# Performance work log

Hardware: AMD Instinct MI355X
Metric: run time of the kernel (lower is better)

The kernel has to match this reference:

```python
import jax, jax.numpy as jnp
import numpy as np

B, T, MAX_ITEMS = 128, 50, 32
NUM_PRODUCT, E, EW = 100000, 128, 16
D = E + EW  # rnn input/hidden size


def setup_inputs() -> dict:
    key = jax.random.key(0)
    ks = jax.random.split(key, 10)
    # items: 0 is padding; keep roughly half the slots padded (ragged baskets)
    items = jax.random.randint(ks[0], (B, T, MAX_ITEMS), 1, NUM_PRODUCT)
    keep = jax.random.uniform(ks[1], (B, T, MAX_ITEMS)) < 0.5
    keep = keep.at[:, :, 0].set(True)  # at least one item per basket
    items = jnp.where(keep, items, 0)
    flag = jax.random.randint(ks[2], (B, T, 1), 0, 2)
    x = jnp.concatenate([items, flag], axis=-1)  # [B,T,MAX_ITEMS+1], last col = flag
    lengths = jnp.full((B,), T, dtype=jnp.int64)
    hidden = jnp.zeros((1, B, D), dtype=jnp.float32)
    s_e = 1.0 / np.sqrt(E)
    s_d = 1.0 / np.sqrt(D)
    encode_w = jax.random.uniform(ks[3], (NUM_PRODUCT, E), minval=-0.1, maxval=0.1)
    encode_w = encode_w.at[0].set(0.0)  # padding_idx=0
    wchange_w = jax.random.normal(ks[4], (2, EW)) * 0.1
    wchange_w = wchange_w.at[0].set(0.0)  # padding_idx=0
    w_ih = jax.random.uniform(ks[5], (3 * D, D), minval=-s_d, maxval=s_d)
    w_hh = jax.random.uniform(ks[6], (3 * D, D), minval=-s_d, maxval=s_d)
    b_ih = jax.random.uniform(ks[7], (3 * D,), minval=-s_d, maxval=s_d)
    b_hh = jax.random.uniform(ks[8], (3 * D,), minval=-s_d, maxval=s_d)
    fc_w = jax.random.uniform(ks[9], (E, D), minval=-s_d, maxval=s_d)
    fc_b = jnp.zeros((E,), dtype=jnp.float32)
    return {"x": x, "lengths": lengths, "hidden": hidden,
            "encode_w": encode_w, "wchange_w": wchange_w,
            "w_ih": w_ih, "w_hh": w_hh, "b_ih": b_ih, "b_hh": b_hh,
            "fc_w": fc_w, "fc_b": fc_b}


def _embed_baskets(x, encode_w, wchange_w):
    items = x[..., :-1]                      # [B,T,I] product ids, 0 = pad
    flag = x[..., -1]                        # [B,T] 0/1 weight-change flag
    emb = encode_w[items]                    # [B,T,I,E] fused ragged gather
    mask = (items != 0).astype(emb.dtype)[..., None]
    cnt = jnp.maximum(mask.sum(axis=2), 1.0)
    pooled = (emb * mask).sum(axis=2) / cnt  # avg pool over real items [B,T,E]
    w = wchange_w[flag]                      # [B,T,EW]
    return jnp.concatenate([pooled, w], axis=-1)  # [B,T,D]


def _gru(seq, h0, w_ih, w_hh, b_ih, b_hh):
    # seq: [B,T,D], h0: [B,D]; torch GRU cell math
    def step(h, x_t):
        gi = x_t @ w_ih.T + b_ih             # [B,3D]
        gh = h @ w_hh.T + b_hh
        i_r, i_z, i_n = jnp.split(gi, 3, axis=-1)
        h_r, h_z, h_n = jnp.split(gh, 3, axis=-1)
        r = jax.nn.sigmoid(i_r + h_r)
        z = jax.nn.sigmoid(i_z + h_z)
        n = jnp.tanh(i_n + r * h_n)
        h_new = (1.0 - z) * n + z * h
        return h_new, h_new
    h_last, outs = jax.lax.scan(step, h0, jnp.swapaxes(seq, 0, 1))
    return jnp.swapaxes(outs, 0, 1), h_last  # [B,T,D], [B,D]


def reference(x, lengths, hidden, encode_w, wchange_w, w_ih, w_hh, b_ih, b_hh, fc_w, fc_b):
    seq = _embed_baskets(x, encode_w, wchange_w)         # [B,T,D]
    out, h_last = _gru(seq, hidden[0], w_ih, w_hh, b_ih, b_hh)
    dynamic_user = out @ fc_w.T + fc_b                   # [B,T,E]
    return dynamic_user, h_last[None]                    # h_u: [1,B,D]
```

## Files before the change

kernel.cpp:

```cpp
#include <hip/hip_runtime.h>
#include <math.h>

#define B_   128
#define T_   50
#define MI_  32
#define E_   128
#define EW_  16
#define D_   144
#define G_   432
#define N_   (B_*T_)

__global__ __launch_bounds__(128) void embed_kernel(
    const int* __restrict__ x,
    const float* __restrict__ encode_w,
    const float* __restrict__ wchange_w,
    float* __restrict__ seq)
{
    int n = blockIdx.x;
    int tid = threadIdx.x;
    __shared__ int xi[33];
    if (tid < 33) xi[tid] = x[n * 33 + tid];
    __syncthreads();

    float acc = 0.f;
    float cnt = 0.f;
    #pragma unroll
    for (int i = 0; i < MI_; ++i) {
        int it = xi[i];
        if (it != 0) {
            cnt += 1.f;
            acc += encode_w[it * E_ + tid];
        }
    }
    seq[n * D_ + tid] = acc / fmaxf(cnt, 1.f);
    if (tid < EW_) {
        int flag = xi[32];
        seq[n * D_ + E_ + tid] = wchange_w[flag * EW_ + tid];
    }
}

#define GK   144
#define GBK  48
#define GPAD 68

__global__ __launch_bounds__(256) void gemm_bias_kernel(
    const float* __restrict__ A,
    const float* __restrict__ Bw,
    const float* __restrict__ bias,
    float* __restrict__ C,
    int M, int N)
{
    __shared__ float As[GBK * GPAD];
    __shared__ float Bs[GBK * GPAD];

    int tid = threadIdx.x;
    int row0 = blockIdx.x * 64;
    int col0 = blockIdx.y * 64;
    int tx = tid & 15;
    int ty = tid >> 4;

    float acc[4][4] = {};

    int sr = tid >> 2;
    int skq0 = tid & 3;

    for (int k0 = 0; k0 < GK; k0 += GBK) {
        __syncthreads();
        #pragma unroll
        for (int i = 0; i < 3; ++i) {
            int kq = skq0 + i * 4;
            float4 a = *(const float4*)&A[(size_t)(row0 + sr) * GK + k0 + kq * 4];
            int nrow = col0 + sr;
            float4 b = make_float4(0.f, 0.f, 0.f, 0.f);
            if (nrow < N)
                b = *(const float4*)&Bw[(size_t)nrow * GK + k0 + kq * 4];
            As[(kq * 4 + 0) * GPAD + sr] = a.x;
            As[(kq * 4 + 1) * GPAD + sr] = a.y;
            As[(kq * 4 + 2) * GPAD + sr] = a.z;
            As[(kq * 4 + 3) * GPAD + sr] = a.w;
            Bs[(kq * 4 + 0) * GPAD + sr] = b.x;
            Bs[(kq * 4 + 1) * GPAD + sr] = b.y;
            Bs[(kq * 4 + 2) * GPAD + sr] = b.z;
            Bs[(kq * 4 + 3) * GPAD + sr] = b.w;
        }
        __syncthreads();

        #pragma unroll 4
        for (int k = 0; k < GBK; ++k) {
            float4 a4 = *(const float4*)&As[k * GPAD + ty * 4];
            float4 b4 = *(const float4*)&Bs[k * GPAD + tx * 4];
            float av[4] = {a4.x, a4.y, a4.z, a4.w};
            float bv[4] = {b4.x, b4.y, b4.z, b4.w};
            #pragma unroll
            for (int i = 0; i < 4; ++i)
                #pragma unroll
                for (int j = 0; j < 4; ++j)
                    acc[i][j] = fmaf(av[i], bv[j], acc[i][j]);
        }
    }

    int c = col0 + tx * 4;
    if (c < N) {
        float4 bb = *(const float4*)&bias[c];
        #pragma unroll
        for (int i = 0; i < 4; ++i) {
            int r = row0 + ty * 4 + i;
            float4 o;
            o.x = acc[i][0] + bb.x;
            o.y = acc[i][1] + bb.y;
            o.z = acc[i][2] + bb.z;
            o.w = acc[i][3] + bb.w;
            *(float4*)&C[(size_t)r * N + c] = o;
        }
    }
}

__global__ __launch_bounds__(448, 1) void gru_kernel(
    const float* __restrict__ gi,
    const float* __restrict__ w_hh,
    const float* __restrict__ b_hh,
    const float* __restrict__ h0,
    float* __restrict__ hseq,
    float* __restrict__ hlast)
{
    int b = blockIdx.x;
    int tid = threadIdx.x;

    __shared__ __align__(16) float h[D_];
    __shared__ float gh[G_];

    int jrow = (tid < G_) ? tid : (G_ - 1);
    float4 w[36];
    #pragma unroll
    for (int i = 0; i < 36; ++i)
        w[i] = *(const float4*)&w_hh[(size_t)jrow * D_ + i * 4];
    float gbias = b_hh[jrow];

    if (tid < D_) h[tid] = h0[b * D_ + tid];
    __syncthreads();

    for (int t = 0; t < T_; ++t) {
        int n = b * T_ + t;
        float gir = 0.f, giz = 0.f, gin = 0.f;
        if (tid < D_) {
            gir = gi[(size_t)n * G_ + tid];
            giz = gi[(size_t)n * G_ + D_ + tid];
            gin = gi[(size_t)n * G_ + 2 * D_ + tid];
        }

        if (tid < G_) {
            float a0 = 0.f, a1 = 0.f, a2 = 0.f, a3 = 0.f;
            #pragma unroll
            for (int i = 0; i < 36; i += 4) {
                float4 hv0 = *(const float4*)&h[(i + 0) * 4];
                float4 hv1 = *(const float4*)&h[(i + 1) * 4];
                float4 hv2 = *(const float4*)&h[(i + 2) * 4];
                float4 hv3 = *(const float4*)&h[(i + 3) * 4];
                a0 = fmaf(w[i + 0].x, hv0.x, a0); a0 = fmaf(w[i + 0].y, hv0.y, a0);
                a0 = fmaf(w[i + 0].z, hv0.z, a0); a0 = fmaf(w[i + 0].w, hv0.w, a0);
                a1 = fmaf(w[i + 1].x, hv1.x, a1); a1 = fmaf(w[i + 1].y, hv1.y, a1);
                a1 = fmaf(w[i + 1].z, hv1.z, a1); a1 = fmaf(w[i + 1].w, hv1.w, a1);
                a2 = fmaf(w[i + 2].x, hv2.x, a2); a2 = fmaf(w[i + 2].y, hv2.y, a2);
                a2 = fmaf(w[i + 2].z, hv2.z, a2); a2 = fmaf(w[i + 2].w, hv2.w, a2);
                a3 = fmaf(w[i + 3].x, hv3.x, a3); a3 = fmaf(w[i + 3].y, hv3.y, a3);
                a3 = fmaf(w[i + 3].z, hv3.z, a3); a3 = fmaf(w[i + 3].w, hv3.w, a3);
            }
            gh[tid] = ((a0 + a1) + (a2 + a3)) + gbias;
        }
        __syncthreads();

        if (tid < D_) {
            float r = 1.f / (1.f + __expf(-(gir + gh[tid])));
            float z = 1.f / (1.f + __expf(-(giz + gh[D_ + tid])));
            float narg = gin + r * gh[2 * D_ + tid];
            narg = fminf(fmaxf(narg, -15.f), 15.f);
            float e2 = __expf(-2.f * narg);
            float nn = (1.f - e2) / (1.f + e2);
            float hn = (1.f - z) * nn + z * h[tid];
            hseq[(size_t)n * D_ + tid] = hn;
            h[tid] = hn;
        }
        __syncthreads();
    }

    if (tid < D_) hlast[b * D_ + tid] = h[tid];
}

extern "C" void kernel_launch(void* const* d_in, const int* in_sizes, int n_in,
                              void* d_out, int out_size, void* d_ws, size_t ws_size,
                              hipStream_t stream)
{
    const int*   x         = (const int*)d_in[0];
    const float* hidden    = (const float*)d_in[2];
    const float* encode_w  = (const float*)d_in[3];
    const float* wchange_w = (const float*)d_in[4];
    const float* w_ih      = (const float*)d_in[5];
    const float* w_hh      = (const float*)d_in[6];
    const float* b_ih      = (const float*)d_in[7];
    const float* b_hh      = (const float*)d_in[8];
    const float* fc_w      = (const float*)d_in[9];
    const float* fc_b      = (const float*)d_in[10];

    float* out = (float*)d_out;
    float* ws  = (float*)d_ws;
    float* seq  = ws;
    float* gi   = ws + 921600;
    float* hseq = ws + 921600 + 2764800;

    embed_kernel<<<N_, 128, 0, stream>>>(x, encode_w, wchange_w, seq);

    gemm_bias_kernel<<<dim3(N_ / 64, (G_ + 63) / 64), 256, 0, stream>>>(
        seq, w_ih, b_ih, gi, N_, G_);

    gru_kernel<<<B_, 448, 0, stream>>>(gi, w_hh, b_hh, hidden, hseq,
                                       out + (size_t)N_ * E_);

    gemm_bias_kernel<<<dim3(N_ / 64, E_ / 64), 256, 0, stream>>>(
        hseq, fc_w, fc_b, out, N_, E_);
}
```

Before: 212.7 us.

## Split GRU recurrent matvec across 8-lane groups with DPP reductions

The recurrent h·W_hh matvec in the GRU kernel is restructured. Instead of one thread computing a full 144-length dot product per gate row, each group of 8 lanes now handles 6 rows, and each lane covers a 20-element slice of k. Partial sums are combined with DPP cross-lane adds, and the block grows from 448 to 576 threads. This shortens the serial per-step FMA chain on the latency-bound recurrence, at the cost of extra reduction instructions, 120 weight registers per thread, and zero-padded k work.

```diff
diff --git a/kernel.cpp b/kernel.cpp
--- a/kernel.cpp
+++ b/kernel.cpp
@@ -115,7 +115,13 @@
     }
 }
 
-__global__ __launch_bounds__(448, 1) void gru_kernel(
+template<int CTRL>
+__device__ __forceinline__ float dpp_xor_add(float x) {
+    int y = __builtin_amdgcn_mov_dpp(__float_as_int(x), CTRL, 0xF, 0xF, true);
+    return x + __int_as_float(y);
+}
+
+__global__ __launch_bounds__(576) void gru_kernel(
     const float* __restrict__ gi,
     const float* __restrict__ w_hh,
     const float* __restrict__ b_hh,
@@ -125,18 +131,31 @@
 {
     int b = blockIdx.x;
     int tid = threadIdx.x;
-
-    __shared__ __align__(16) float h[D_];
+    int g = tid >> 3;
+    int s = tid & 7;
+    int k0 = s * 20;
+
+    __shared__ __align__(16) float h[160];
     __shared__ float gh[G_];
 
-    int jrow = (tid < G_) ? tid : (G_ - 1);
-    float4 w[36];
+    float w[6][20];
     #pragma unroll
-    for (int i = 0; i < 36; ++i)
-        w[i] = *(const float4*)&w_hh[(size_t)jrow * D_ + i * 4];
-    float gbias = b_hh[jrow];
-
-    if (tid < D_) h[tid] = h0[b * D_ + tid];
+    for (int r = 0; r < 6; ++r) {
+        const float* wrow = &w_hh[(size_t)(6 * g + r) * D_];
+        #pragma unroll
+        for (int q = 0; q < 5; ++q) {
+            int k = k0 + 4 * q;
+            float4 t = make_float4(0.f, 0.f, 0.f, 0.f);
+            if (k < D_) t = *(const float4*)&wrow[k];
+            w[r][4 * q + 0] = t.x;
+            w[r][4 * q + 1] = t.y;
+            w[r][4 * q + 2] = t.z;
+            w[r][4 * q + 3] = t.w;
+        }
+    }
+    float bias = (s < 6) ? b_hh[6 * g + s] : 0.f;
+
+    if (tid < 160) h[tid] = (tid < D_) ? h0[b * D_ + tid] : 0.f;
     __syncthreads();
 
     for (int t = 0; t < T_; ++t) {
@@ -148,25 +167,42 @@
             gin = gi[(size_t)n * G_ + 2 * D_ + tid];
         }
 
-        if (tid < G_) {
-            float a0 = 0.f, a1 = 0.f, a2 = 0.f, a3 = 0.f;
-            #pragma unroll
-            for (int i = 0; i < 36; i += 4) {
-                float4 hv0 = *(const float4*)&h[(i + 0) * 4];
-                float4 hv1 = *(const float4*)&h[(i + 1) * 4];
-                float4 hv2 = *(const float4*)&h[(i + 2) * 4];
-                float4 hv3 = *(const float4*)&h[(i + 3) * 4];
-                a0 = fmaf(w[i + 0].x, hv0.x, a0); a0 = fmaf(w[i + 0].y, hv0.y, a0);
-                a0 = fmaf(w[i + 0].z, hv0.z, a0); a0 = fmaf(w[i + 0].w, hv0.w, a0);
-                a1 = fmaf(w[i + 1].x, hv1.x, a1); a1 = fmaf(w[i + 1].y, hv1.y, a1);
-                a1 = fmaf(w[i + 1].z, hv1.z, a1); a1 = fmaf(w[i + 1].w, hv1.w, a1);
-                a2 = fmaf(w[i + 2].x, hv2.x, a2); a2 = fmaf(w[i + 2].y, hv2.y, a2);
-                a2 = fmaf(w[i + 2].z, hv2.z, a2); a2 = fmaf(w[i + 2].w, hv2.w, a2);
-                a3 = fmaf(w[i + 3].x, hv3.x, a3); a3 = fmaf(w[i + 3].y, hv3.y, a3);
-                a3 = fmaf(w[i + 3].z, hv3.z, a3); a3 = fmaf(w[i + 3].w, hv3.w, a3);
-            }
-            gh[tid] = ((a0 + a1) + (a2 + a3)) + gbias;
-        }
+        float hv[20];
+        #pragma unroll
+        for (int q = 0; q < 5; ++q) {
+            float4 t4 = *(const float4*)&h[k0 + 4 * q];
+            hv[4 * q + 0] = t4.x;
+            hv[4 * q + 1] = t4.y;
+            hv[4 * q + 2] = t4.z;
+            hv[4 * q + 3] = t4.w;
+        }
+
+        float a0 = 0.f, a1 = 0.f, a2 = 0.f, a3 = 0.f, a4 = 0.f, a5 = 0.f;
+        #pragma unroll
+        for (int kk = 0; kk < 20; ++kk) {
+            float hk = hv[kk];
+            a0 = fmaf(w[0][kk], hk, a0);
+            a1 = fmaf(w[1][kk], hk, a1);
+            a2 = fmaf(w[2][kk], hk, a2);
+            a3 = fmaf(w[3][kk], hk, a3);
+            a4 = fmaf(w[4][kk], hk, a4);
+            a5 = fmaf(w[5][kk], hk, a5);
+        }
+
+        a0 = dpp_xor_add<0xB1>(a0); a0 = dpp_xor_add<0x4E>(a0); a0 = dpp_xor_add<0x141>(a0);
+        a1 = dpp_xor_add<0xB1>(a1); a1 = dpp_xor_add<0x4E>(a1); a1 = dpp_xor_add<0x141>(a1);
+        a2 = dpp_xor_add<0xB1>(a2); a2 = dpp_xor_add<0x4E>(a2); a2 = dpp_xor_add<0x141>(a2);
+        a3 = dpp_xor_add<0xB1>(a3); a3 = dpp_xor_add<0x4E>(a3); a3 = dpp_xor_add<0x141>(a3);
+        a4 = dpp_xor_add<0xB1>(a4); a4 = dpp_xor_add<0x4E>(a4); a4 = dpp_xor_add<0x141>(a4);
+        a5 = dpp_xor_add<0xB1>(a5); a5 = dpp_xor_add<0x4E>(a5); a5 = dpp_xor_add<0x141>(a5);
+
+        float myacc = a0;
+        if (s == 1) myacc = a1;
+        if (s == 2) myacc = a2;
+        if (s == 3) myacc = a3;
+        if (s == 4) myacc = a4;
+        if (s == 5) myacc = a5;
+        if (s < 6) gh[6 * g + s] = myacc + bias;
         __syncthreads();
 
         if (tid < D_) {
@@ -212,7 +248,7 @@
     gemm_bias_kernel<<<dim3(N_ / 64, (G_ + 63) / 64), 256, 0, stream>>>(
         seq, w_ih, b_ih, gi, N_, G_);
 
-    gru_kernel<<<B_, 448, 0, stream>>>(gi, w_hh, b_hh, hidden, hseq,
+    gru_kernel<<<B_, 576, 0, stream>>>(gi, w_hh, b_hh, hidden, hseq,
                                        out + (size_t)N_ * E_);
 
     gemm_bias_kernel<<<dim3(N_ / 64, E_ / 64), 256, 0, stream>>>(
```

Result: faster. 194.5 us (-8.6%).
